# Kernel tuning notes

Measured on AMD Instinct MI355X. Metric: run time of the kernel, lower is better.

## Reference

```python
import jax, jax.numpy as jnp
import numpy as np

LN2 = 0.6931471805599453
BLOCK_SIZE = 16
MANT_BITS = 7  # HybridLowBlockFP(BLOCK_SIZE, 8, 7, 7): 8-bit signed mantissa, shared block exponent
Q_MAGIC = np.int16(24375)  # bf16 Quake rsqrt magic constant from isqrt_sftm


def _quake_rsqrt(x):
    """Bit-trick bfloat16 rsqrt seed + one Newton iteration (matches isqrt_sftm)."""
    y_bf = x.astype(jnp.bfloat16)
    i = jax.lax.bitcast_convert_type(y_bf, jnp.int16)
    i = Q_MAGIC - (i >> 1)
    y = jax.lax.bitcast_convert_type(i, jnp.bfloat16).astype(x.dtype)
    x_half = x * 0.5
    # y_out = y * (1.5 - 0.5*x*y*y)
    return y * (1.5 - (x_half * y) * y)


def _bfp_quant(x, block_size=BLOCK_SIZE, mant_bits=MANT_BITS):
    """Block floating point: shared exponent per block of `block_size` along last dim,
    signed (mant_bits+1)-bit mantissa."""
    shp = x.shape
    xb = x.reshape(shp[:-1] + (shp[-1] // block_size, block_size))
    maxabs = jnp.max(jnp.abs(xb), axis=-1, keepdims=True)
    safe = jnp.where(maxabs > 0, maxabs, 1.0)
    shared_exp = jnp.floor(jnp.log2(safe)) + 1.0        # mantissa of max in [2^(m-1), 2^m)
    scale = jnp.exp2(shared_exp - mant_bits)
    qmax = float(2 ** mant_bits - 1)
    q = jnp.clip(jnp.round(xb / scale), -float(2 ** mant_bits), qmax) * scale
    q = jnp.where(maxabs > 0, q, 0.0)
    return q.reshape(shp)


def setup_inputs() -> dict:
    key = jax.random.key(0)
    x = jax.random.normal(key, (1, 16, 2048, 2048), dtype=jnp.float32)
    return {"x": x}


def reference(x) -> jnp.ndarray:
    # power-of-two exp approximation: exp(x) ~= 2^floor(x/ln2)
    q = jnp.floor(x / LN2)
    exp_x = jnp.exp2(q)
    exp_x_sum = jnp.sum(exp_x, axis=-1, keepdims=True)  # [B,H,S,1]
    rs = _quake_rsqrt(exp_x_sum)                        # ~ 1/sqrt(sum)
    div_out = (exp_x * rs) * rs                         # exp_x / sum via rsqrt^2
    return _bfp_quant(div_out.astype(jnp.float32))
```

## Files before the change

kernel.cpp:

```cpp
#include <hip/hip_runtime.h>
#include <cstdint>


#define LN2F 0.69314718055994530942f
#define COLS 2048

__global__ __launch_bounds__(256) void hmq_softmax_kernel(
    const float* __restrict__ x, float* __restrict__ out) {
    const int tid = threadIdx.x;
    const int rowLocal = tid >> 7;
    const int lane128 = tid & 127;
    const long long row = (long long)blockIdx.x * 2 + rowLocal;
    const float* xr = x + row * COLS;
    float* outr = out + row * COLS;

    float4 xin[4];
#pragma unroll
    for (int k = 0; k < 4; ++k)
        xin[k] = reinterpret_cast<const float4*>(xr)[lane128 + 128 * k];

    const double INV_LN2_D = 1.0 / (double)LN2F;
    float e[16];
    float psum = 0.0f;
#pragma unroll
    for (int k = 0; k < 4; ++k) {
        float xs[4] = {xin[k].x, xin[k].y, xin[k].z, xin[k].w};
#pragma unroll
        for (int j = 0; j < 4; ++j) {
            float qr = (float)((double)xs[j] * INV_LN2_D);
            int qi = (int)floorf(qr);
            float ev = __uint_as_float((uint32_t)(qi + 127) << 23);
            e[k * 4 + j] = ev;
            psum += ev;
        }
    }

    float wsum = psum;
#pragma unroll
    for (int off = 1; off < 64; off <<= 1)
        wsum += __shfl_xor(wsum, off, 64);

    __shared__ float lds[4];
    const int wave = tid >> 6;
    if ((tid & 63) == 0) lds[wave] = wsum;
    __syncthreads();
    const float s = lds[rowLocal * 2] + lds[rowLocal * 2 + 1];

    uint32_t ub = __float_as_uint(s);
    uint32_t lsb = (ub >> 16) & 1u;
    uint16_t bbits = (uint16_t)((ub + 0x7FFFu + lsb) >> 16);
    int16_t ii = (int16_t)bbits;
    ii = (int16_t)(24375 - (ii >> 1));
    float y = __uint_as_float(((uint32_t)(uint16_t)ii) << 16);
    float xh = __fmul_rn(s, 0.5f);
    float t = __fmul_rn(__fmul_rn(xh, y), y);
    float r = __fsub_rn(1.5f, t);
    float rs = __fmul_rn(y, r);

#pragma unroll
    for (int k = 0; k < 4; ++k) {
        float v[4];
        float m = 0.0f;
#pragma unroll
        for (int j = 0; j < 4; ++j) {
            v[j] = __fmul_rn(__fmul_rn(e[k * 4 + j], rs), rs);
            m = fmaxf(m, v[j]);
        }
        m = fmaxf(m, __shfl_xor(m, 1, 64));
        m = fmaxf(m, __shfl_xor(m, 2, 64));
        int ex = (int)((__float_as_uint(m) >> 23) & 0xFFu) - 126;
        float scale = __uint_as_float((uint32_t)(ex - 7 + 127) << 23);
        float inv_scale = __uint_as_float((uint32_t)(7 - ex + 127) << 23);
        float4 o;
        float* op = &o.x;
#pragma unroll
        for (int j = 0; j < 4; ++j) {
            float qv = rintf(__fmul_rn(v[j], inv_scale));
            qv = fminf(fmaxf(qv, -128.0f), 127.0f);
            op[j] = __fmul_rn(qv, scale);
        }
        reinterpret_cast<float4*>(outr)[lane128 + 128 * k] = o;
    }
}

extern "C" void kernel_launch(void* const* d_in, const int* in_sizes, int n_in,
                              void* d_out, int out_size, void* d_ws, size_t ws_size,
                              hipStream_t stream) {
    const float* x = (const float*)d_in[0];
    float* out = (float*)d_out;
    const long long total = in_sizes[0];
    const int nrows = (int)(total / COLS);
    const int grid = nrows / 2;
    hmq_softmax_kernel<<<grid, 256, 0, stream>>>(x, out);
}
```

Measured before the change: 97.09 us.

## Map one wave per row, drop LDS reduction, use nontemporal loads/stores

Each 64-lane wave now owns a full 2048-element row, so the row sum is reduced with wave shuffles alone and the shared-memory exchange and __syncthreads are removed. Each thread holds 8 float4 values instead of 4, which raises register use, and each block covers 4 rows. Loads and stores use nontemporal builtins to avoid polluting cache on this streaming, memory-bound kernel. floorf plus int conversion is replaced by a round-down conversion intrinsic.

```diff
diff --git a/kernel.cpp b/kernel.cpp
--- a/kernel.cpp
+++ b/kernel.cpp
@@ -5,46 +5,40 @@
 #define LN2F 0.69314718055994530942f
 #define COLS 2048
 
+typedef float f32x4 __attribute__((ext_vector_type(4)));
+
 __global__ __launch_bounds__(256) void hmq_softmax_kernel(
     const float* __restrict__ x, float* __restrict__ out) {
     const int tid = threadIdx.x;
-    const int rowLocal = tid >> 7;
-    const int lane128 = tid & 127;
-    const long long row = (long long)blockIdx.x * 2 + rowLocal;
-    const float* xr = x + row * COLS;
-    float* outr = out + row * COLS;
+    const int wave = tid >> 6;
+    const int lane = tid & 63;
+    const long long row = (long long)blockIdx.x * 4 + wave;
+    const f32x4* xr = reinterpret_cast<const f32x4*>(x + row * COLS);
+    f32x4* outr = reinterpret_cast<f32x4*>(out + row * COLS);
 
-    float4 xin[4];
+    f32x4 d[8];
 #pragma unroll
-    for (int k = 0; k < 4; ++k)
-        xin[k] = reinterpret_cast<const float4*>(xr)[lane128 + 128 * k];
+    for (int k = 0; k < 8; ++k)
+        d[k] = __builtin_nontemporal_load(&xr[lane + 64 * k]);
 
     const double INV_LN2_D = 1.0 / (double)LN2F;
-    float e[16];
     float psum = 0.0f;
 #pragma unroll
-    for (int k = 0; k < 4; ++k) {
-        float xs[4] = {xin[k].x, xin[k].y, xin[k].z, xin[k].w};
+    for (int k = 0; k < 8; ++k) {
 #pragma unroll
         for (int j = 0; j < 4; ++j) {
-            float qr = (float)((double)xs[j] * INV_LN2_D);
-            int qi = (int)floorf(qr);
+            float qr = (float)((double)d[k][j] * INV_LN2_D);
+            int qi = __float2int_rd(qr);
             float ev = __uint_as_float((uint32_t)(qi + 127) << 23);
-            e[k * 4 + j] = ev;
+            d[k][j] = ev;
             psum += ev;
         }
     }
 
-    float wsum = psum;
+    float s = psum;
 #pragma unroll
     for (int off = 1; off < 64; off <<= 1)
-        wsum += __shfl_xor(wsum, off, 64);
-
-    __shared__ float lds[4];
-    const int wave = tid >> 6;
-    if ((tid & 63) == 0) lds[wave] = wsum;
-    __syncthreads();
-    const float s = lds[rowLocal * 2] + lds[rowLocal * 2 + 1];
+        s += __shfl_xor(s, off, 64);
 
     uint32_t ub = __float_as_uint(s);
     uint32_t lsb = (ub >> 16) & 1u;
@@ -58,28 +52,26 @@
     float rs = __fmul_rn(y, r);
 
 #pragma unroll
-    for (int k = 0; k < 4; ++k) {
-        float v[4];
+    for (int k = 0; k < 8; ++k) {
         float m = 0.0f;
 #pragma unroll
         for (int j = 0; j < 4; ++j) {
-            v[j] = __fmul_rn(__fmul_rn(e[k * 4 + j], rs), rs);
-            m = fmaxf(m, v[j]);
+            d[k][j] = __fmul_rn(__fmul_rn(d[k][j], rs), rs);
+            m = fmaxf(m, d[k][j]);
         }
         m = fmaxf(m, __shfl_xor(m, 1, 64));
         m = fmaxf(m, __shfl_xor(m, 2, 64));
         int ex = (int)((__float_as_uint(m) >> 23) & 0xFFu) - 126;
         float scale = __uint_as_float((uint32_t)(ex - 7 + 127) << 23);
         float inv_scale = __uint_as_float((uint32_t)(7 - ex + 127) << 23);
-        float4 o;
-        float* op = &o.x;
+        f32x4 o;
 #pragma unroll
         for (int j = 0; j < 4; ++j) {
-            float qv = rintf(__fmul_rn(v[j], inv_scale));
+            float qv = rintf(__fmul_rn(d[k][j], inv_scale));
             qv = fminf(fmaxf(qv, -128.0f), 127.0f);
-            op[j] = __fmul_rn(qv, scale);
+            o[j] = __fmul_rn(qv, scale);
         }
-        reinterpret_cast<float4*>(outr)[lane128 + 128 * k] = o;
+        __builtin_nontemporal_store(o, &outr[lane + 64 * k]);
     }
 }
 
@@ -90,6 +82,6 @@
     float* out = (float*)d_out;
     const long long total = in_sizes[0];
     const int nrows = (int)(total / COLS);
-    const int grid = nrows / 2;
+    const int grid = nrows / 4;
     hmq_softmax_kernel<<<grid, 256, 0, stream>>>(x, out);
 }
```

After: 90.61 us. 6.7% less time.
